# Optimization experiments

Measured on AMD Instinct MI355X. Metric: run time of the kernel, lower is better.

Reference implementation:

```python
import jax, jax.numpy as jnp
import numpy as np

N = 100000
E = 1600000
IN_C = 128
HID = 128
NUM_CLASSES = 16


def setup_inputs() -> dict:
    key = jax.random.key(0)
    ks = jax.random.split(key, 8)
    x = jax.random.normal(ks[0], (N, IN_C), dtype=jnp.float32)
    edge_index = jax.random.randint(ks[1], (2, E), 0, N, dtype=jnp.int64)
    s1 = 1.0 / np.sqrt(IN_C)
    s2 = 1.0 / np.sqrt(HID)
    W1 = jax.random.uniform(ks[2], (IN_C, HID), jnp.float32, -s1, s1)
    b1 = jnp.zeros((HID,), jnp.float32)
    W2 = jax.random.uniform(ks[3], (HID, HID), jnp.float32, -s2, s2)
    b2 = jnp.zeros((HID,), jnp.float32)
    Wl = jax.random.uniform(ks[4], (HID, NUM_CLASSES), jnp.float32, -s2, s2)
    bl = jax.random.uniform(ks[5], (NUM_CLASSES,), jnp.float32, -s2, s2)
    return {"x": x, "edge_index": edge_index, "W1": W1, "b1": b1,
            "W2": W2, "b2": b2, "Wl": Wl, "bl": bl}


def gcn_conv(x, src, dst, norm, W, b, n_nodes):
    # x: [N, F_in]; src/dst: [E+N] (self-loops appended); norm: [E+N]
    h = x @ W  # [N, F_out] -- transform first (F_out <= F_in style), then gather
    msg = h[src] * norm[:, None]  # [E+N, F_out] gathered, normalized messages
    out = jax.ops.segment_sum(msg, dst, num_segments=n_nodes)  # scatter-add
    return out + b


def reference(x, edge_index, W1, b1, W2, b2, Wl, bl):
    loop = jnp.arange(N, dtype=edge_index.dtype)
    src = jnp.concatenate([edge_index[0], loop])  # add self-loops
    dst = jnp.concatenate([edge_index[1], loop])
    # symmetric GCN normalization: deg computed on target side incl. self-loops
    deg = jax.ops.segment_sum(jnp.ones_like(dst, dtype=x.dtype), dst,
                              num_segments=N)
    dinv = jnp.where(deg > 0, jax.lax.rsqrt(deg), 0.0)
    norm = dinv[src] * dinv[dst]  # [E+N]

    h = jax.nn.relu(gcn_conv(x, src, dst, norm, W1, b1, N))
    h = jax.nn.relu(gcn_conv(h, src, dst, norm, W2, b2, N))
    logits = h @ Wl + bl
    return jax.nn.softmax(logits, axis=1)
```

## Files before the change

### kernel.cpp

```cpp
#include <hip/hip_runtime.h>
#include <hip/hip_fp16.h>

#define FDIM 128
#define NCLS 16

#define SCAN_T 256
#define SCAN_I 8
#define SCAN_CHUNK (SCAN_T * SCAN_I)

typedef _Float16 f16x8 __attribute__((ext_vector_type(8)));
typedef float f32x4 __attribute__((ext_vector_type(4)));

__global__ void k_count(const int* __restrict__ dst, int* cnt, int e) {
    int i = blockIdx.x * blockDim.x + threadIdx.x;
    if (i < e) atomicAdd(&cnt[dst[i]], 1);
}

__global__ __launch_bounds__(SCAN_T) void k_scan1(const int* __restrict__ cnt,
                                                  int* __restrict__ excl,
                                                  int* __restrict__ blockSum,
                                                  float* __restrict__ dinv, int n) {
    __shared__ int ts[SCAN_T];
    int b = blockIdx.x, t = threadIdx.x;
    int base = b * SCAN_CHUNK + t * SCAN_I;
    int v[SCAN_I];
    int s = 0;
    #pragma unroll
    for (int i = 0; i < SCAN_I; ++i) {
        int idx = base + i;
        v[i] = (idx < n) ? cnt[idx] : 0;
        if (idx < n) dinv[idx] = rsqrtf((float)(v[i] + 1));
        s += v[i];
    }
    ts[t] = s;
    __syncthreads();
    for (int off = 1; off < SCAN_T; off <<= 1) {
        int x = (t >= off) ? ts[t - off] : 0;
        __syncthreads();
        ts[t] += x;
        __syncthreads();
    }
    int ex = (t == 0) ? 0 : ts[t - 1];
    #pragma unroll
    for (int i = 0; i < SCAN_I; ++i) {
        int idx = base + i;
        if (idx < n) excl[idx] = ex;
        ex += v[i];
    }
    if (t == SCAN_T - 1) blockSum[b] = ts[SCAN_T - 1];
}

__global__ __launch_bounds__(1024) void k_scan2_prepw(int* blockSum, int* total, int nb,
                                                      const float* __restrict__ W1,
                                                      const float* __restrict__ W2,
                                                      __half* __restrict__ T1,
                                                      __half* __restrict__ T2) {
    if (blockIdx.x == 0) {
        __shared__ int ts[1024];
        int t = threadIdx.x;
        int v = (t < nb) ? blockSum[t] : 0;
        ts[t] = v;
        __syncthreads();
        for (int off = 1; off < 1024; off <<= 1) {
            int x = (t >= off) ? ts[t - off] : 0;
            __syncthreads();
            ts[t] += x;
            __syncthreads();
        }
        if (t < nb) blockSum[t] = (t == 0) ? 0 : ts[t - 1];
        if (t == 1023) *total = ts[1023];
    } else {
        const float* W = (blockIdx.x == 1) ? W1 : W2;
        __half* T = (blockIdx.x == 1) ? T1 : T2;
        for (int i = threadIdx.x; i < 128 * 32; i += 1024) {
            int c = i >> 5, k4 = (i & 31) * 4;
            float a = W[(k4 + 0) * 128 + c];
            float b = W[(k4 + 1) * 128 + c];
            float d = W[(k4 + 2) * 128 + c];
            float f = W[(k4 + 3) * 128 + c];
            __half2 h0 = __float22half2_rn(make_float2(a, b));
            __half2 h1 = __float22half2_rn(make_float2(d, f));
            uint2 u;
            u.x = *reinterpret_cast<unsigned int*>(&h0);
            u.y = *reinterpret_cast<unsigned int*>(&h1);
            *reinterpret_cast<uint2*>(&T[c * 128 + k4]) = u;
        }
    }
}

__global__ void k_scan3(int* __restrict__ row_ptr, int* __restrict__ cursor,
                        const int* __restrict__ blockSum, const int* __restrict__ total,
                        int n) {
    int i = blockIdx.x * blockDim.x + threadIdx.x;
    if (i < n) {
        int v = row_ptr[i] + blockSum[i / SCAN_CHUNK];
        row_ptr[i] = v;
        cursor[i] = v;
    }
    if (i == 0) row_ptr[n] = *total;
}

__global__ void k_scatter(const int* __restrict__ src, const int* __restrict__ dst,
                          int* cursor, int* __restrict__ csr_off, int e) {
    int i = blockIdx.x * blockDim.x + threadIdx.x;
    if (i >= e) return;
    int pos = atomicAdd(&cursor[dst[i]], 1);
    csr_off[pos] = src[i] << 8;
}

template <typename T>
__global__ __launch_bounds__(512) void k_gemm_mfma(const T* __restrict__ A,
                                                   const __half* __restrict__ WT,
                                                   const float* __restrict__ dinv,
                                                   __half* __restrict__ C, int n) {
    __shared__ _Float16 as[128 * 128];
    __shared__ _Float16 wt[128 * 128];
    int t = threadIdx.x;
    int r0 = blockIdx.x * 128;

    for (int i = t; i < 2048; i += 512) {
        int c = i >> 4, k8 = i & 15;
        uint4 u = reinterpret_cast<const uint4*>(WT)[i];
        int byte = (c * 256 + k8 * 16) ^ ((c & 7) << 4);
        *reinterpret_cast<uint4*>(reinterpret_cast<char*>(wt) + byte) = u;
    }

    if constexpr (sizeof(T) == 4) {
        for (int i = t; i < 128 * 16; i += 512) {
            int r = i >> 4, c8 = i & 15;
            float4 v0 = make_float4(0.f, 0.f, 0.f, 0.f);
            float4 v1 = make_float4(0.f, 0.f, 0.f, 0.f);
            if (r0 + r < n) {
                v0 = reinterpret_cast<const float4*>(A)[(size_t)(r0 + r) * 32 + c8 * 2];
                v1 = reinterpret_cast<const float4*>(A)[(size_t)(r0 + r) * 32 + c8 * 2 + 1];
            }
            __half2 h0 = __float22half2_rn(make_float2(v0.x, v0.y));
            __half2 h1 = __float22half2_rn(make_float2(v0.z, v0.w));
            __half2 h2 = __float22half2_rn(make_float2(v1.x, v1.y));
            __half2 h3 = __float22half2_rn(make_float2(v1.z, v1.w));
            uint4 u;
            u.x = *reinterpret_cast<unsigned int*>(&h0);
            u.y = *reinterpret_cast<unsigned int*>(&h1);
            u.z = *reinterpret_cast<unsigned int*>(&h2);
            u.w = *reinterpret_cast<unsigned int*>(&h3);
            int byte = (r * 256 + c8 * 16) ^ ((r & 7) << 4);
            *reinterpret_cast<uint4*>(reinterpret_cast<char*>(as) + byte) = u;
        }
    } else {
        for (int i = t; i < 128 * 16; i += 512) {
            int r = i >> 4, c8 = i & 15;
            uint4 u = make_uint4(0, 0, 0, 0);
            if (r0 + r < n)
                u = reinterpret_cast<const uint4*>(A)[(size_t)(r0 + r) * 16 + c8];
            int byte = (r * 256 + c8 * 16) ^ ((r & 7) << 4);
            *reinterpret_cast<uint4*>(reinterpret_cast<char*>(as) + byte) = u;
        }
    }
    __syncthreads();

    int w = t >> 6, l = t & 63;
    int lrow = l & 15, lk = l >> 4;
    int rw = w * 16;

    f16x8 afrag[4];
    #pragma unroll
    for (int ks = 0; ks < 4; ++ks) {
        int row = rw + lrow;
        int byte = (row * 256 + (ks * 4 + lk) * 16) ^ ((row & 7) << 4);
        afrag[ks] = *reinterpret_cast<const f16x8*>(reinterpret_cast<const char*>(as) + byte);
    }
    float dv[4];
    #pragma unroll
    for (int reg = 0; reg < 4; ++reg) {
        int rg = r0 + rw + lk * 4 + reg;
        dv[reg] = (rg < n) ? dinv[rg] : 0.f;
    }

    #pragma unroll
    for (int ct = 0; ct < 8; ++ct) {
        f32x4 acc = {0.f, 0.f, 0.f, 0.f};
        #pragma unroll
        for (int ks = 0; ks < 4; ++ks) {
            int c = ct * 16 + lrow;
            int byte = (c * 256 + (ks * 4 + lk) * 16) ^ ((c & 7) << 4);
            f16x8 bfrag = *reinterpret_cast<const f16x8*>(reinterpret_cast<const char*>(wt) + byte);
            acc = __builtin_amdgcn_mfma_f32_16x16x32_f16(afrag[ks], bfrag, acc, 0, 0, 0);
        }
        #pragma unroll
        for (int reg = 0; reg < 4; ++reg) {
            int rg = r0 + rw + lk * 4 + reg;
            if (rg < n)
                C[(size_t)rg * FDIM + ct * 16 + lrow] = __float2half(acc[reg] * dv[reg]);
        }
    }
}

template <bool FUSE>
__global__ __launch_bounds__(256) void k_agg2e(const __half* __restrict__ Y,
                                               const int* __restrict__ csr_off,
                                               const int* __restrict__ row_ptr,
                                               const float* __restrict__ dinv,
                                               const float* __restrict__ bias,
                                               const float* __restrict__ Wl,
                                               const float* __restrict__ bl,
                                               __half* __restrict__ hout,
                                               float* __restrict__ out, int n) {
    __shared__ float s_wl[NCLS * FDIM];
    __shared__ float s_bl[NCLS];
    if (FUSE) {
        for (int i = threadIdx.x; i < FDIM * NCLS / 4; i += 256) {
            int k = i >> 2, c4 = (i & 3) * 4;
            float4 v = reinterpret_cast<const float4*>(Wl)[i];
            s_wl[(c4 + 0) * FDIM + k] = v.x;
            s_wl[(c4 + 1) * FDIM + k] = v.y;
            s_wl[(c4 + 2) * FDIM + k] = v.z;
            s_wl[(c4 + 3) * FDIM + k] = v.w;
        }
        if (threadIdx.x < NCLS) s_bl[threadIdx.x] = bl[threadIdx.x];
        __syncthreads();
    }

    int node = blockIdx.x * 4 + (threadIdx.x >> 6);
    if (node >= n) return;
    int lane = threadIdx.x & 63;
    int half = lane >> 5, l32 = lane & 31;
    const char* Yb = reinterpret_cast<const char*>(Y);
    const char* lanebase = Yb + (l32 << 3);

    float a0 = 0.f, a1 = 0.f, a2 = 0.f, a3 = 0.f;
    int beg = row_ptr[node], end = row_ptr[node + 1];

    for (int j0 = beg; j0 < end; j0 += 64) {
        int cnt = min(64, end - j0);
        int myoff = (j0 + lane < end) ? csr_off[j0 + lane] : 0;
        int k = 0;
        for (; k + 8 <= cnt; k += 8) {
            uint2 u[4];
            #pragma unroll
            for (int i = 0; i < 4; ++i) {
                int oe = __builtin_amdgcn_readlane(myoff, k + 2 * i);
                int oo = __builtin_amdgcn_readlane(myoff, k + 2 * i + 1);
                int off = half ? oo : oe;
                u[i] = *reinterpret_cast<const uint2*>(lanebase + off);
            }
            __half2* p = reinterpret_cast<__half2*>(u);
            __half2 lo = __hadd2(__hadd2(p[0], p[2]), __hadd2(p[4], p[6]));
            __half2 hi = __hadd2(__hadd2(p[1], p[3]), __hadd2(p[5], p[7]));
            float2 flo = __half22float2(lo), fhi = __half22float2(hi);
            a0 += flo.x; a1 += flo.y; a2 += fhi.x; a3 += fhi.y;
        }
        for (; k + 2 <= cnt; k += 2) {
            int oe = __builtin_amdgcn_readlane(myoff, k);
            int oo = __builtin_amdgcn_readlane(myoff, k + 1);
            int off = half ? oo : oe;
            uint2 u = *reinterpret_cast<const uint2*>(lanebase + off);
            __half2* p = reinterpret_cast<__half2*>(&u);
            float2 flo = __half22float2(p[0]), fhi = __half22float2(p[1]);
            a0 += flo.x; a1 += flo.y; a2 += fhi.x; a3 += fhi.y;
        }
        if (k < cnt) {
            int o = __builtin_amdgcn_readlane(myoff, k);
            uint2 u = *reinterpret_cast<const uint2*>(lanebase + o);
            __half2* p = reinterpret_cast<__half2*>(&u);
            float sel = (half == 0) ? 1.0f : 0.0f;
            float2 flo = __half22float2(p[0]), fhi = __half22float2(p[1]);
            a0 += flo.x * sel; a1 += flo.y * sel;
            a2 += fhi.x * sel; a3 += fhi.y * sel;
        }
    }

    a0 += __shfl_xor(a0, 32, 64);
    a1 += __shfl_xor(a1, 32, 64);
    a2 += __shfl_xor(a2, 32, 64);
    a3 += __shfl_xor(a3, 32, 64);

    uint2 su = *reinterpret_cast<const uint2*>(Yb + ((size_t)node << 8) + (l32 << 3));
    __half2* sp = reinterpret_cast<__half2*>(&su);
    float2 slo = __half22float2(sp[0]), shi = __half22float2(sp[1]);
    a0 += slo.x; a1 += slo.y; a2 += shi.x; a3 += shi.y;

    float di = dinv[node];
    float4 b = *reinterpret_cast<const float4*>(bias + l32 * 4);
    float h0 = fmaxf(a0 * di + b.x, 0.f);
    float h1 = fmaxf(a1 * di + b.y, 0.f);
    float h2 = fmaxf(a2 * di + b.z, 0.f);
    float h3 = fmaxf(a3 * di + b.w, 0.f);

    if (!FUSE) {
        if (half == 0) {
            __half2 o0 = __float22half2_rn(make_float2(h0, h1));
            __half2 o1 = __float22half2_rn(make_float2(h2, h3));
            uint2 o;
            o.x = *reinterpret_cast<unsigned int*>(&o0);
            o.y = *reinterpret_cast<unsigned int*>(&o1);
            *reinterpret_cast<uint2*>(reinterpret_cast<char*>(hout) + ((size_t)node << 8) + (l32 << 3)) = o;
        }
    } else {
        float lg[NCLS];
        #pragma unroll
        for (int c = 0; c < NCLS; ++c) {
            float4 w4 = *reinterpret_cast<const float4*>(&s_wl[c * FDIM + l32 * 4]);
            lg[c] = h0 * w4.x + h1 * w4.y + h2 * w4.z + h3 * w4.w;
        }
        #pragma unroll
        for (int off = 1; off < 32; off <<= 1) {
            #pragma unroll
            for (int c = 0; c < NCLS; ++c) lg[c] += __shfl_xor(lg[c], off, 64);
        }
        #pragma unroll
        for (int c = 0; c < NCLS; ++c) lg[c] += s_bl[c];
        float m = lg[0];
        #pragma unroll
        for (int c = 1; c < NCLS; ++c) m = fmaxf(m, lg[c]);
        float ev[NCLS];
        float sum = 0.f;
        #pragma unroll
        for (int c = 0; c < NCLS; ++c) { ev[c] = __expf(lg[c] - m); sum += ev[c]; }
        float inv = 1.0f / sum;
        float mye = 0.f;
        #pragma unroll
        for (int c = 0; c < NCLS; ++c) if (lane == c) mye = ev[c];
        if (lane < NCLS) out[(size_t)node * NCLS + lane] = mye * inv;
    }
}

extern "C" void kernel_launch(void* const* d_in, const int* in_sizes, int n_in,
                              void* d_out, int out_size, void* d_ws, size_t ws_size,
                              hipStream_t stream) {
    const float* x  = (const float*)d_in[0];
    const int*   ei = (const int*)d_in[1];
    const float* W1 = (const float*)d_in[2];
    const float* b1 = (const float*)d_in[3];
    const float* W2 = (const float*)d_in[4];
    const float* b2 = (const float*)d_in[5];
    const float* Wl = (const float*)d_in[6];
    const float* bl = (const float*)d_in[7];
    float* out = (float*)d_out;

    int n = in_sizes[0] / FDIM;
    int e = in_sizes[1] / 2;
    const int* src = ei;
    const int* dst = ei + e;

    int nb = (n + SCAN_CHUNK - 1) / SCAN_CHUNK;

    float* dinv    = (float*)d_ws;
    int*   cnt     = (int*)(dinv + n);
    int*   row_ptr = cnt + n;
    int*   cursor  = row_ptr + n + 1;
    int*   blockSum= cursor + n;
    int*   total   = blockSum + 1024;
    int*   csr_off = total + 1;
    uintptr_t p = (uintptr_t)(csr_off + e);
    p = (p + 15) & ~(uintptr_t)15;
    __half* wt1 = (__half*)p;
    __half* wt2 = wt1 + 128 * 128;
    __half* bufA = wt2 + 128 * 128;
    __half* bufB = bufA + (size_t)n * FDIM;

    int bn = (n + 255) / 256;
    int be = (e + 255) / 256;

    hipMemsetAsync(cnt, 0, (size_t)n * sizeof(int), stream);
    k_count<<<be, 256, 0, stream>>>(dst, cnt, e);
    k_scan1<<<nb, SCAN_T, 0, stream>>>(cnt, row_ptr, blockSum, dinv, n);
    k_scan2_prepw<<<3, 1024, 0, stream>>>(blockSum, total, nb, W1, W2, wt1, wt2);
    k_scan3<<<bn, 256, 0, stream>>>(row_ptr, cursor, blockSum, total, n);
    k_scatter<<<be, 256, 0, stream>>>(src, dst, cursor, csr_off, e);

    int bg = (n + 127) / 128;
    int ba = (n + 3) / 4;

    k_gemm_mfma<float><<<bg, 512, 0, stream>>>(x, wt1, dinv, bufA, n);
    k_agg2e<false><<<ba, 256, 0, stream>>>(bufA, csr_off, row_ptr, dinv, b1, Wl, bl, bufB, out, n);

    k_gemm_mfma<__half><<<bg, 512, 0, stream>>>(bufB, wt2, dinv, bufA, n);
    k_agg2e<true><<<ba, 256, 0, stream>>>(bufA, csr_off, row_ptr, dinv, b2, Wl, bl, bufB, out, n);
}
```

Baseline: 461.5 us.

## Two-pass bucketed CSR scatter to localize atomic cursor writes

Replaces the single random scatter of edges into CSR with a two-pass scheme. The first pass partitions edges by coarse destination bucket (up to 64 buckets) through shared-memory staging and writes (src,dst) pairs contiguously per bucket. The second pass then does the per-node atomic cursor increment and CSR write over bucket-ordered edges, so the atomics and stores land in a smaller, more cache-resident region. In exchange it adds an extra kernel and an extra read and write of an 8-byte-per-edge pairs array.

```diff
diff --git a/kernel.cpp b/kernel.cpp
--- a/kernel.cpp
+++ b/kernel.cpp
@@ -7,6 +7,9 @@
 #define SCAN_T 256
 #define SCAN_I 8
 #define SCAN_CHUNK (SCAN_T * SCAN_I)
+
+#define EPB 4096
+#define MAXBUK 64
 
 typedef _Float16 f16x8 __attribute__((ext_vector_type(8)));
 typedef float f32x4 __attribute__((ext_vector_type(4)));
@@ -90,22 +93,68 @@
 
 __global__ void k_scan3(int* __restrict__ row_ptr, int* __restrict__ cursor,
                         const int* __restrict__ blockSum, const int* __restrict__ total,
-                        int n) {
+                        int* __restrict__ bcur, int shift, int n) {
     int i = blockIdx.x * blockDim.x + threadIdx.x;
     if (i < n) {
         int v = row_ptr[i] + blockSum[i / SCAN_CHUNK];
         row_ptr[i] = v;
         cursor[i] = v;
+        if ((i & ((1 << shift) - 1)) == 0) bcur[i >> shift] = v;
     }
     if (i == 0) row_ptr[n] = *total;
 }
 
-__global__ void k_scatter(const int* __restrict__ src, const int* __restrict__ dst,
-                          int* cursor, int* __restrict__ csr_off, int e) {
+__global__ __launch_bounds__(512) void k_bucket(const int* __restrict__ src,
+                                                const int* __restrict__ dst,
+                                                int* bcur, uint2* __restrict__ pairs,
+                                                int e, int shift, int nbuk) {
+    __shared__ int hist[MAXBUK], lhist[MAXBUK], base[MAXBUK], lpre[MAXBUK];
+    __shared__ uint2 slab[EPB];
+    __shared__ unsigned char bkt[EPB];
+    int t = threadIdx.x;
+    int e0 = blockIdx.x * EPB;
+    int cntE = min(EPB, e - e0);
+
+    if (t < nbuk) { hist[t] = 0; lhist[t] = 0; }
+    __syncthreads();
+
+    for (int k = t; k < cntE; k += 512) {
+        int b = dst[e0 + k] >> shift;
+        atomicAdd(&hist[b], 1);
+    }
+    __syncthreads();
+
+    if (t < nbuk) base[t] = atomicAdd(&bcur[t], hist[t]);
+    if (t == 0) {
+        int acc = 0;
+        for (int b = 0; b < nbuk; ++b) { lpre[b] = acc; acc += hist[b]; }
+    }
+    __syncthreads();
+
+    for (int k = t; k < cntE; k += 512) {
+        int d = dst[e0 + k];
+        int s = src[e0 + k];
+        int b = d >> shift;
+        int r = atomicAdd(&lhist[b], 1);
+        int j = lpre[b] + r;
+        slab[j] = make_uint2((unsigned)(s << 8), (unsigned)d);
+        bkt[j] = (unsigned char)b;
+    }
+    __syncthreads();
+
+    for (int j = t; j < cntE; j += 512) {
+        int b = bkt[j];
+        pairs[base[b] + (j - lpre[b])] = slab[j];
+    }
+}
+
+__global__ void k_fine(const uint2* __restrict__ pairs, int* cursor,
+                       int* __restrict__ csr_off, int e) {
     int i = blockIdx.x * blockDim.x + threadIdx.x;
     if (i >= e) return;
-    int pos = atomicAdd(&cursor[dst[i]], 1);
-    csr_off[pos] = src[i] << 8;
+    uint2 up = pairs[i];
+    int pos = atomicAdd(&cursor[up.y], 1);
+    csr_off[pos] = (int)up.x;
 }
 
 template <typename T>
@@ -344,16 +393,22 @@
 
     int nb = (n + SCAN_CHUNK - 1) / SCAN_CHUNK;
 
+    int shift = 11;
+    while (((n + (1 << shift) - 1) >> shift) > MAXBUK) ++shift;
+    int nbuk = (n + (1 << shift) - 1) >> shift;
+
     float* dinv    = (float*)d_ws;
     int*   cnt     = (int*)(dinv + n);
     int*   row_ptr = cnt + n;
     int*   cursor  = row_ptr + n + 1;
     int*   blockSum= cursor + n;
     int*   total   = blockSum + 1024;
-    int*   csr_off = total + 1;
+    int*   bcur    = total + 1;
+    int*   csr_off = bcur + MAXBUK;
     uintptr_t p = (uintptr_t)(csr_off + e);
     p = (p + 15) & ~(uintptr_t)15;
-    __half* wt1 = (__half*)p;
+    uint2* pairs = (uint2*)p;
+    __half* wt1 = (__half*)(pairs + e);
     __half* wt2 = wt1 + 128 * 128;
     __half* bufA = wt2 + 128 * 128;
     __half* bufB = bufA + (size_t)n * FDIM;
@@ -365,8 +420,11 @@
     k_count<<<be, 256, 0, stream>>>(dst, cnt, e);
     k_scan1<<<nb, SCAN_T, 0, stream>>>(cnt, row_ptr, blockSum, dinv, n);
     k_scan2_prepw<<<3, 1024, 0, stream>>>(blockSum, total, nb, W1, W2, wt1, wt2);
-    k_scan3<<<bn, 256, 0, stream>>>(row_ptr, cursor, blockSum, total, n);
-    k_scatter<<<be, 256, 0, stream>>>(src, dst, cursor, csr_off, e);
+    k_scan3<<<bn, 256, 0, stream>>>(row_ptr, cursor, blockSum, total, bcur, shift, n);
+
+    int bbk = (e + EPB - 1) / EPB;
+    k_bucket<<<bbk, 512, 0, stream>>>(src, dst, bcur, pairs, e, shift, nbuk);
+    k_fine<<<be, 256, 0, stream>>>(pairs, cursor, csr_off, e);
 
     int bg = (n + 127) / 128;
     int ba = (n + 3) / 4;
```

Measured after the change: 421.4 us (median of 2 runs). 1.1x faster.
